# Performance work log

Measured on AMD Instinct MI355X. Metric: run time of the kernel, lower is better.

The kernel has to match this reference:

```python
import jax, jax.numpy as jnp
import numpy as np

N, E, B = 50000, 500000, 500
NODE_IN, EDGE_IN = 64, 16
NODE_OUT, EDGE_OUT = 96, 64
FP_DIM, FP_EMBED = 2048, 128
HIDDEN = [512, 512]
OUT = 256
BN_EPS = 1e-5


def setup_inputs() -> dict:
    key = jax.random.key(0)
    ks = jax.random.split(key, 16)
    inp = {
        "node_feats": jax.random.normal(ks[0], (N, NODE_IN), jnp.float32),
        "edge_feats": jax.random.normal(ks[1], (E, EDGE_IN), jnp.float32),
        "fp_vector": jax.random.uniform(ks[2], (B, FP_DIM), jnp.float32),
        "src": jax.random.randint(ks[3], (E,), 0, N, dtype=jnp.int32),
        "dst": jax.random.randint(ks[4], (E,), 0, N, dtype=jnp.int32),
        "graph_ids": jnp.sort(jax.random.randint(ks[5], (N,), 0, B, dtype=jnp.int32)),
        # mpnn stand-in: single node projection
        "W_mpnn": jax.random.normal(ks[6], (NODE_IN, NODE_OUT), jnp.float32) / np.sqrt(NODE_IN),
        "b_mpnn": jnp.zeros((NODE_OUT,), jnp.float32),
        # project_edge_feats_module: linear edge projection
        "W_edge": jax.random.normal(ks[7], (EDGE_IN, EDGE_OUT), jnp.float32) / np.sqrt(EDGE_IN),
        "b_edge": jnp.zeros((EDGE_OUT,), jnp.float32),
        # FingerprintEncoder: Linear + BatchNorm1d (eval) + ReLU (+Dropout off)
        "W_fp": jax.random.normal(ks[8], (FP_DIM, FP_EMBED), jnp.float32) / np.sqrt(FP_DIM),
        "b_fp": jnp.zeros((FP_EMBED,), jnp.float32),
        "bn_gamma": jnp.ones((FP_EMBED,), jnp.float32),
        "bn_beta": jnp.zeros((FP_EMBED,), jnp.float32),
        "bn_mean": jnp.zeros((FP_EMBED,), jnp.float32),
        "bn_var": jnp.ones((FP_EMBED,), jnp.float32),
    }
    d_in = NODE_OUT + EDGE_OUT + FP_EMBED  # gnn_readout_dim + fp_embed_dim
    dims = [d_in] + HIDDEN + [OUT]
    for i in range(len(dims) - 1):
        inp[f"W_ffn{i}"] = jax.random.normal(ks[9 + i], (dims[i], dims[i + 1]), jnp.float32) / np.sqrt(dims[i])
        inp[f"b_ffn{i}"] = jnp.zeros((dims[i + 1],), jnp.float32)
    return inp


def reference(node_feats, edge_feats, fp_vector, src, dst, graph_ids,
              W_mpnn, b_mpnn, W_edge, b_edge,
              W_fp, b_fp, bn_gamma, bn_beta, bn_mean, bn_var,
              W_ffn0, b_ffn0, W_ffn1, b_ffn1, W_ffn2, b_ffn2):
    # mpnn node encodings [N, NODE_OUT]
    node_emb = node_feats @ W_mpnn + b_mpnn
    # projected edge embeddings [E, EDGE_OUT]
    edge_emb = edge_feats @ W_edge + b_edge
    # message: gather src node emb, concat edge emb -> [E, NODE_OUT+EDGE_OUT]
    msg = jnp.concatenate([node_emb[src], edge_emb], axis=1)
    # reduce: sum messages per destination node -> [N, NODE_OUT+EDGE_OUT]
    node_msg_sum = jax.ops.segment_sum(msg, dst, num_segments=N)
    # global_sum_pooling over nodes per graph -> [B, NODE_OUT+EDGE_OUT]
    mol = jax.ops.segment_sum(node_msg_sum, graph_ids, num_segments=B)
    mol = jax.nn.softmax(mol, axis=1)
    # fingerprint encoder (eval mode: BN uses running stats, dropout off)
    fp = fp_vector @ W_fp + b_fp
    fp = (fp - bn_mean) * jax.lax.rsqrt(bn_var + BN_EPS) * bn_gamma + bn_beta
    fp = jax.nn.relu(fp)
    # combined FFN (dropout off in eval)
    x = jnp.concatenate([mol, fp], axis=1)
    x = jax.nn.relu(x @ W_ffn0 + b_ffn0)
    x = jax.nn.relu(x @ W_ffn1 + b_ffn1)
    return x @ W_ffn2 + b_ffn2
```

## Files before the change

### kernel.cpp

```cpp
#include <hip/hip_runtime.h>
#include <math.h>

#define NODE_IN 64
#define NODE_OUT 96
#define EDGE_IN 16
#define EDGE_OUT 64
#define ACC_W 80
#define NB 500
#define FPD 2048
#define FPE 128
#define XDIM 288
#define BN_EPS 1e-5f
#define HB 2048

__global__ __launch_bounds__(256) void hist_kernel(
    const int* __restrict__ dst, const int* __restrict__ gids,
    int* __restrict__ gkey, int* __restrict__ pbh, int E)
{
    __shared__ int h[NB];
    const int t = threadIdx.x;
    for (int i = t; i < NB; i += 256) h[i] = 0;
    __syncthreads();
    const int e0 = blockIdx.x * HB;
    #pragma unroll
    for (int i = 0; i < HB / 256; ++i) {
        const int e = e0 + i * 256 + t;
        if (e < E) {
            const int g = gids[dst[e]];
            gkey[e] = g;
            atomicAdd(&h[g], 1);
        }
    }
    __syncthreads();
    for (int i = t; i < NB; i += 256)
        pbh[(size_t)blockIdx.x * NB + i] = h[i];
}

__global__ __launch_bounds__(256) void colscan_kernel(
    const int* __restrict__ pbh, int* __restrict__ pcs,
    int* __restrict__ gsum, int nblk)
{
    __shared__ int s[256];
    const int g = blockIdx.x;
    const int t = threadIdx.x;
    const int v0 = (t < nblk) ? pbh[(size_t)t * NB + g] : 0;
    s[t] = v0;
    __syncthreads();
    for (int d = 1; d < 256; d <<= 1) {
        const int v = (t >= d) ? s[t - d] : 0;
        __syncthreads();
        s[t] += v;
        __syncthreads();
    }
    if (t < nblk) pcs[(size_t)t * NB + g] = s[t] - v0;
    if (t == 255) gsum[g] = s[255];
}

__global__ __launch_bounds__(512) void gscan_kernel(
    const int* __restrict__ gsum, int* __restrict__ offs, int* __restrict__ tot)
{
    __shared__ int s[512];
    const int t = threadIdx.x;
    const int v0 = (t < NB) ? gsum[t] : 0;
    s[t] = v0;
    __syncthreads();
    for (int d = 1; d < 512; d <<= 1) {
        const int v = (t >= d) ? s[t - d] : 0;
        __syncthreads();
        s[t] += v;
        __syncthreads();
    }
    if (t < NB) {
        offs[t] = s[t] - v0;
        tot[t]  = v0;
    }
}

__global__ __launch_bounds__(256) void scatter2_kernel(
    const int* __restrict__ gkey, const int* __restrict__ src,
    const int* __restrict__ pcs, const int* __restrict__ offs,
    int* __restrict__ ssrc, int* __restrict__ seid, int E)
{
    __shared__ int h[NB];
    __shared__ int basel[NB];
    const int t = threadIdx.x;
    for (int i = t; i < NB; i += 256) {
        h[i] = 0;
        basel[i] = offs[i] + pcs[(size_t)blockIdx.x * NB + i];
    }
    __syncthreads();
    const int e0 = blockIdx.x * HB;
    #pragma unroll
    for (int i = 0; i < HB / 256; ++i) {
        const int e = e0 + i * 256 + t;
        if (e < E) {
            const int g = gkey[e];
            const int r = atomicAdd(&h[g], 1);
            const int p = basel[g] + r;
            ssrc[p] = src[e];
            seid[p] = e;
        }
    }
}

__global__ __launch_bounds__(1024) void graph_accum(
    const int* __restrict__ ssrc, const int* __restrict__ seid,
    const float* __restrict__ nf, const float* __restrict__ ef,
    const int* __restrict__ offs, const int* __restrict__ tot,
    const float* __restrict__ Wm, const float* __restrict__ bm,
    const float* __restrict__ We, const float* __restrict__ be,
    float* __restrict__ xbuf, int E)
{
    const int g = blockIdx.x;
    const int t = threadIdx.x;
    const int lane = t & 63;
    const int w = t >> 6;
    const int start = offs[g];
    const int cnt = tot[g];
    const int end = start + cnt;
    const int q = lane >> 4, c = lane & 15;

    __shared__ float sacc[16][ACC_W];
    __shared__ float accRow[ACC_W];
    __shared__ float red[1024];

    float nacc = 0.f;
    float eacc = 0.f;

    for (int p0 = start + w * 64; p0 < end; p0 += 1024) {
        const int lim = min(64, end - p0);
        const int sv = ssrc[min(p0 + lane, E - 1)];
        const int ev = seid[min(p0 + lane, E - 1)];

        #pragma unroll
        for (int u0 = 0; u0 < 64; u0 += 16) {
            float v[16];
            #pragma unroll
            for (int u = 0; u < 16; ++u) {
                const int s = __builtin_amdgcn_readlane(sv, u0 + u);
                v[u] = nf[(size_t)s * NODE_IN + lane];
            }
            #pragma unroll
            for (int u = 0; u < 16; ++u)
                nacc += (u0 + u < lim) ? v[u] : 0.f;
        }

        #pragma unroll
        for (int u0 = 0; u0 < 16; u0 += 8) {
            float w8[8];
            int idx8[8];
            #pragma unroll
            for (int u = 0; u < 8; ++u) {
                const int idx = (u0 + u) * 4 + q;
                const int eid = __shfl(ev, idx);
                idx8[u] = idx;
                w8[u] = ef[(size_t)eid * EDGE_IN + c];
            }
            #pragma unroll
            for (int u = 0; u < 8; ++u)
                eacc += (idx8[u] < lim) ? w8[u] : 0.f;
        }
    }

    if (lane < NODE_IN) sacc[w][lane] = nacc;
    eacc += __shfl_xor(eacc, 16);
    eacc += __shfl_xor(eacc, 32);
    if (lane < EDGE_IN) sacc[w][NODE_IN + lane] = eacc;
    __syncthreads();
    if (t < ACC_W) {
        float s = 0.f;
        #pragma unroll
        for (int w2 = 0; w2 < 16; ++w2) s += sacc[w2][t];
        accRow[t] = s;
    }
    __syncthreads();

    const float cntf = (float)cnt;
    float mr = 0.f;
    if (t < 96) {
        float m2 = 0.f;
        for (int k = 0; k < NODE_IN; ++k) m2 = fmaf(accRow[k], Wm[k * NODE_OUT + t], m2);
        mr = m2 + cntf * bm[t];
    } else if (t < 160) {
        const int j = t - 96;
        float m2 = 0.f;
        for (int k = 0; k < EDGE_IN; ++k) m2 = fmaf(accRow[NODE_IN + k], We[k * EDGE_OUT + j], m2);
        mr = m2 + cntf * be[j];
    }

    red[t] = (t < 160) ? mr : -1e30f;
    __syncthreads();
    for (int st = 512; st > 0; st >>= 1) {
        if (t < st) red[t] = fmaxf(red[t], red[t + st]);
        __syncthreads();
    }
    const float mx = red[0];
    __syncthreads();
    const float evx = (t < 160) ? expf(mr - mx) : 0.f;
    red[t] = evx;
    __syncthreads();
    for (int st = 512; st > 0; st >>= 1) {
        if (t < st) red[t] += red[t + st];
        __syncthreads();
    }
    if (t < 160) xbuf[(size_t)g * XDIM + t] = evx / red[0];
}

__global__ __launch_bounds__(1024) void fp_kernel(
    const float* __restrict__ fpv, const float* __restrict__ Wf,
    const float* __restrict__ bf, const float* __restrict__ gam,
    const float* __restrict__ bet, const float* __restrict__ mu,
    const float* __restrict__ var, float* __restrict__ xbuf)
{
    __shared__ float part[7][4][FPE];
    const int t = threadIdx.x;
    const int j  = t & 127;
    const int kh = __builtin_amdgcn_readfirstlane(t >> 7);
    const int r0 = blockIdx.x * 4;
    const int k0 = kh * 256;

    const float* __restrict__ xp0 = fpv + (size_t)(r0 + 0) * FPD + k0;
    const float* __restrict__ xp1 = fpv + (size_t)(r0 + 1) * FPD + k0;
    const float* __restrict__ xp2 = fpv + (size_t)(r0 + 2) * FPD + k0;
    const float* __restrict__ xp3 = fpv + (size_t)(r0 + 3) * FPD + k0;
    const float* __restrict__ wp  = Wf + (size_t)k0 * FPE + j;

    float a0 = 0.f, a1 = 0.f, a2 = 0.f, a3 = 0.f;
    for (int k = 0; k < 256; k += 8) {
        #pragma unroll
        for (int u = 0; u < 8; ++u) {
            const float w = wp[(size_t)(k + u) * FPE];
            a0 = fmaf(xp0[k + u], w, a0);
            a1 = fmaf(xp1[k + u], w, a1);
            a2 = fmaf(xp2[k + u], w, a2);
            a3 = fmaf(xp3[k + u], w, a3);
        }
    }
    if (kh > 0) {
        part[kh - 1][0][j] = a0; part[kh - 1][1][j] = a1;
        part[kh - 1][2][j] = a2; part[kh - 1][3][j] = a3;
    }
    __syncthreads();
    if (kh == 0) {
        #pragma unroll
        for (int qd = 0; qd < 7; ++qd) {
            a0 += part[qd][0][j]; a1 += part[qd][1][j];
            a2 += part[qd][2][j]; a3 += part[qd][3][j];
        }
        const float sc = rsqrtf(var[j] + BN_EPS) * gam[j];
        const float sh = bet[j] - mu[j] * sc;
        const float bj = bf[j];
        xbuf[(size_t)(r0 + 0) * XDIM + 160 + j] = fmaxf(fmaf(a0 + bj, sc, sh), 0.f);
        xbuf[(size_t)(r0 + 1) * XDIM + 160 + j] = fmaxf(fmaf(a1 + bj, sc, sh), 0.f);
        xbuf[(size_t)(r0 + 2) * XDIM + 160 + j] = fmaxf(fmaf(a2 + bj, sc, sh), 0.f);
        xbuf[(size_t)(r0 + 3) * XDIM + 160 + j] = fmaxf(fmaf(a3 + bj, sc, sh), 0.f);
    }
}

template<int NO, int KS>
__global__ __launch_bounds__(1024) void ffn_split(
    const float* __restrict__ X, const float* __restrict__ W,
    const float* __restrict__ bias, float* __restrict__ Y,
    int Bv, int Ni, int doRelu)
{
    __shared__ float part[KS - 1][4][NO];
    const int t = threadIdx.x;
    const int col = t % NO;
    const int ks = __builtin_amdgcn_readfirstlane(t / NO);
    const int r0 = blockIdx.x * 4;
    const int kchunk = Ni / KS;
    const int k0 = ks * kchunk;

    const float* __restrict__ xp0 = X + (size_t)(r0 + 0) * Ni + k0;
    const float* __restrict__ xp1 = X + (size_t)(r0 + 1) * Ni + k0;
    const float* __restrict__ xp2 = X + (size_t)(r0 + 2) * Ni + k0;
    const float* __restrict__ xp3 = X + (size_t)(r0 + 3) * Ni + k0;
    const float* __restrict__ wp  = W + (size_t)k0 * NO + col;

    float a0 = 0.f, a1 = 0.f, a2 = 0.f, a3 = 0.f;
    for (int k = 0; k < kchunk; k += 8) {
        #pragma unroll
        for (int u = 0; u < 8; ++u) {
            const float w = wp[(size_t)(k + u) * NO];
            a0 = fmaf(xp0[k + u], w, a0);
            a1 = fmaf(xp1[k + u], w, a1);
            a2 = fmaf(xp2[k + u], w, a2);
            a3 = fmaf(xp3[k + u], w, a3);
        }
    }
    if (ks > 0) {
        part[ks - 1][0][col] = a0; part[ks - 1][1][col] = a1;
        part[ks - 1][2][col] = a2; part[ks - 1][3][col] = a3;
    }
    __syncthreads();
    if (ks == 0) {
        #pragma unroll
        for (int qd = 0; qd < KS - 1; ++qd) {
            a0 += part[qd][0][col]; a1 += part[qd][1][col];
            a2 += part[qd][2][col]; a3 += part[qd][3][col];
        }
        const float bv = bias[col];
        float o0 = a0 + bv, o1 = a1 + bv, o2 = a2 + bv, o3 = a3 + bv;
        if (doRelu) {
            o0 = fmaxf(o0, 0.f); o1 = fmaxf(o1, 0.f);
            o2 = fmaxf(o2, 0.f); o3 = fmaxf(o3, 0.f);
        }
        Y[(size_t)(r0 + 0) * NO + col] = o0;
        if (r0 + 1 < Bv) Y[(size_t)(r0 + 1) * NO + col] = o1;
        if (r0 + 2 < Bv) Y[(size_t)(r0 + 2) * NO + col] = o2;
        if (r0 + 3 < Bv) Y[(size_t)(r0 + 3) * NO + col] = o3;
    }
}

extern "C" void kernel_launch(void* const* d_in, const int* in_sizes, int n_in,
                              void* d_out, int out_size, void* d_ws, size_t ws_size,
                              hipStream_t stream)
{
    const float* node_feats = (const float*)d_in[0];
    const float* edge_feats = (const float*)d_in[1];
    const float* fpv        = (const float*)d_in[2];
    const int*   src        = (const int*)d_in[3];
    const int*   dst        = (const int*)d_in[4];
    const int*   gids       = (const int*)d_in[5];
    const float* Wm  = (const float*)d_in[6];
    const float* bm  = (const float*)d_in[7];
    const float* We  = (const float*)d_in[8];
    const float* be  = (const float*)d_in[9];
    const float* Wf  = (const float*)d_in[10];
    const float* bf  = (const float*)d_in[11];
    const float* gam = (const float*)d_in[12];
    const float* bet = (const float*)d_in[13];
    const float* mu  = (const float*)d_in[14];
    const float* var = (const float*)d_in[15];
    const float* W0  = (const float*)d_in[16];
    const float* b0  = (const float*)d_in[17];
    const float* W1  = (const float*)d_in[18];
    const float* b1  = (const float*)d_in[19];
    const float* W2  = (const float*)d_in[20];
    const float* b2  = (const float*)d_in[21];
    const int E = in_sizes[3];
    const int nblk = (E + HB - 1) / HB;

    float* xbuf  = (float*)d_ws;
    float* h1    = xbuf + (size_t)NB * XDIM;
    float* h2    = h1 + (size_t)NB * 512;
    int*   gkey  = (int*)(h2 + (size_t)NB * 512);
    int*   ssrc  = gkey + E;
    int*   seid  = ssrc + E;
    int*   pbh   = seid + E;
    int*   pcs   = pbh + (size_t)nblk * NB;
    int*   gsum  = pcs + (size_t)nblk * NB;
    int*   offs  = gsum + NB;
    int*   tot   = offs + NB;

    hipLaunchKernelGGL(hist_kernel, dim3(nblk), dim3(256), 0, stream,
                       dst, gids, gkey, pbh, E);
    hipLaunchKernelGGL(colscan_kernel, dim3(NB), dim3(256), 0, stream,
                       pbh, pcs, gsum, nblk);
    hipLaunchKernelGGL(gscan_kernel, dim3(1), dim3(512), 0, stream,
                       gsum, offs, tot);
    hipLaunchKernelGGL(scatter2_kernel, dim3(nblk), dim3(256), 0, stream,
                       gkey, src, pcs, offs, ssrc, seid, E);
    hipLaunchKernelGGL(graph_accum, dim3(NB), dim3(1024), 0, stream,
                       ssrc, seid, node_feats, edge_feats, offs, tot,
                       Wm, bm, We, be, xbuf, E);
    hipLaunchKernelGGL(fp_kernel, dim3(NB / 4), dim3(1024), 0, stream,
                       fpv, Wf, bf, gam, bet, mu, var, xbuf);
    hipLaunchKernelGGL((ffn_split<512, 2>), dim3((NB + 3) / 4), dim3(1024), 0, stream,
                       xbuf, W0, b0, h1, NB, XDIM, 1);
    hipLaunchKernelGGL((ffn_split<512, 2>), dim3((NB + 3) / 4), dim3(1024), 0, stream,
                       h1, W1, b1, h2, NB, 512, 1);
    hipLaunchKernelGGL((ffn_split<256, 4>), dim3((NB + 3) / 4), dim3(1024), 0, stream,
                       h2, W2, b2, (float*)d_out, NB, 512, 0);
}
```

Measured before the change: 113.6 us.

## Accumulate edge features per graph in histogram pass and fuse fingerprint encoder

The histogram kernel now streams edge features contiguously and accumulates them into per-block, per-graph shared-memory partial sums, written to a new workspace buffer. This removes the sorted edge-id array and the random gather of edge features in the graph accumulation kernel. The fingerprint encoder is merged into the graph accumulation launch as extra blocks, saving one kernel launch and letting the two overlap. In exchange it adds shared-memory float atomics, a 32KB shared array per histogram block, and a strided reduction over all block partials for each graph.

```diff
diff --git a/kernel.cpp b/kernel.cpp
--- a/kernel.cpp
+++ b/kernel.cpp
@@ -13,27 +13,51 @@
 #define BN_EPS 1e-5f
 #define HB 2048
 
-__global__ __launch_bounds__(256) void hist_kernel(
+__global__ __launch_bounds__(512) void hist_kernel(
     const int* __restrict__ dst, const int* __restrict__ gids,
-    int* __restrict__ gkey, int* __restrict__ pbh, int E)
-{
-    __shared__ int h[NB];
-    const int t = threadIdx.x;
-    for (int i = t; i < NB; i += 256) h[i] = 0;
-    __syncthreads();
+    const float* __restrict__ ef,
+    int* __restrict__ gkey, int* __restrict__ pbh, float* __restrict__ pfe, int E)
+{
+    __shared__ int   h[NB];
+    __shared__ float facc[NB * EDGE_IN];
+    const int t = threadIdx.x;
+    for (int i = t; i < NB; i += 512) h[i] = 0;
+    for (int i = t; i < NB * EDGE_IN; i += 512) facc[i] = 0.f;
+    __syncthreads();
+
+    const int lane = t & 63;
+    const int w = t >> 6;
+    const int q = lane >> 4, c = lane & 15;
     const int e0 = blockIdx.x * HB;
-    #pragma unroll
-    for (int i = 0; i < HB / 256; ++i) {
-        const int e = e0 + i * 256 + t;
+
+    for (int b = w; b < HB / 64; b += 8) {
+        const int eb = e0 + b * 64;
+        const int e = eb + lane;
+        int g = -1;
         if (e < E) {
-            const int g = gids[dst[e]];
+            g = gids[dst[e]];
             gkey[e] = g;
             atomicAdd(&h[g], 1);
         }
-    }
-    __syncthreads();
-    for (int i = t; i < NB; i += 256)
+        #pragma unroll
+        for (int k0 = 0; k0 < 16; k0 += 8) {
+            float v[8]; int gq[8];
+            #pragma unroll
+            for (int u = 0; u < 8; ++u) {
+                const int idx = (k0 + u) * 4 + q;
+                gq[u] = __shfl(g, idx);
+                v[u] = (gq[u] >= 0) ? ef[(size_t)(eb + idx) * EDGE_IN + c] : 0.f;
+            }
+            #pragma unroll
+            for (int u = 0; u < 8; ++u)
+                if (gq[u] >= 0) atomicAdd(&facc[gq[u] * EDGE_IN + c], v[u]);
+        }
+    }
+    __syncthreads();
+    for (int i = t; i < NB; i += 512)
         pbh[(size_t)blockIdx.x * NB + i] = h[i];
+    for (int i = t; i < NB * EDGE_IN; i += 512)
+        pfe[(size_t)blockIdx.x * (NB * EDGE_IN) + i] = facc[i];
 }
 
 __global__ __launch_bounds__(256) void colscan_kernel(
@@ -76,62 +100,115 @@
     }
 }
 
-__global__ __launch_bounds__(256) void scatter2_kernel(
+__global__ __launch_bounds__(512) void scatter2_kernel(
     const int* __restrict__ gkey, const int* __restrict__ src,
     const int* __restrict__ pcs, const int* __restrict__ offs,
-    int* __restrict__ ssrc, int* __restrict__ seid, int E)
+    int* __restrict__ ssrc, int E)
 {
     __shared__ int h[NB];
     __shared__ int basel[NB];
     const int t = threadIdx.x;
-    for (int i = t; i < NB; i += 256) {
+    for (int i = t; i < NB; i += 512) {
         h[i] = 0;
         basel[i] = offs[i] + pcs[(size_t)blockIdx.x * NB + i];
     }
     __syncthreads();
     const int e0 = blockIdx.x * HB;
     #pragma unroll
-    for (int i = 0; i < HB / 256; ++i) {
-        const int e = e0 + i * 256 + t;
+    for (int i = 0; i < HB / 512; ++i) {
+        const int e = e0 + i * 512 + t;
         if (e < E) {
             const int g = gkey[e];
             const int r = atomicAdd(&h[g], 1);
-            const int p = basel[g] + r;
-            ssrc[p] = src[e];
-            seid[p] = e;
-        }
-    }
-}
-
-__global__ __launch_bounds__(1024) void graph_accum(
-    const int* __restrict__ ssrc, const int* __restrict__ seid,
-    const float* __restrict__ nf, const float* __restrict__ ef,
-    const int* __restrict__ offs, const int* __restrict__ tot,
+            ssrc[basel[g] + r] = src[e];
+        }
+    }
+}
+
+__global__ __launch_bounds__(1024) void fused_kernel(
+    const int* __restrict__ ssrc, const float* __restrict__ nf,
+    const float* __restrict__ pfe, const int* __restrict__ offs,
+    const int* __restrict__ tot, int nblk,
     const float* __restrict__ Wm, const float* __restrict__ bm,
     const float* __restrict__ We, const float* __restrict__ be,
+    const float* __restrict__ fpv, const float* __restrict__ Wf,
+    const float* __restrict__ bf, const float* __restrict__ gam,
+    const float* __restrict__ bet, const float* __restrict__ mu,
+    const float* __restrict__ var,
     float* __restrict__ xbuf, int E)
 {
+    __shared__ float sacc[16][NODE_IN];
+    __shared__ float epart[16][EDGE_IN];
+    __shared__ float accRow[ACC_W];
+    __shared__ float red[1024];
+    __shared__ float part[7][4][FPE];
+
+    const int t = threadIdx.x;
+
+    if (blockIdx.x >= NB) {
+        const int j  = t & 127;
+        const int kh = __builtin_amdgcn_readfirstlane(t >> 7);
+        const int r0 = (blockIdx.x - NB) * 4;
+        const int k0 = kh * 256;
+
+        const float* __restrict__ xp0 = fpv + (size_t)(r0 + 0) * FPD + k0;
+        const float* __restrict__ xp1 = fpv + (size_t)(r0 + 1) * FPD + k0;
+        const float* __restrict__ xp2 = fpv + (size_t)(r0 + 2) * FPD + k0;
+        const float* __restrict__ xp3 = fpv + (size_t)(r0 + 3) * FPD + k0;
+        const float* __restrict__ wp  = Wf + (size_t)k0 * FPE + j;
+
+        float a0 = 0.f, a1 = 0.f, a2 = 0.f, a3 = 0.f;
+        for (int k = 0; k < 256; k += 8) {
+            #pragma unroll
+            for (int u = 0; u < 8; ++u) {
+                const float w = wp[(size_t)(k + u) * FPE];
+                a0 = fmaf(xp0[k + u], w, a0);
+                a1 = fmaf(xp1[k + u], w, a1);
+                a2 = fmaf(xp2[k + u], w, a2);
+                a3 = fmaf(xp3[k + u], w, a3);
+            }
+        }
+        if (kh > 0) {
+            part[kh - 1][0][j] = a0; part[kh - 1][1][j] = a1;
+            part[kh - 1][2][j] = a2; part[kh - 1][3][j] = a3;
+        }
+        __syncthreads();
+        if (kh == 0) {
+            #pragma unroll
+            for (int qd = 0; qd < 7; ++qd) {
+                a0 += part[qd][0][j]; a1 += part[qd][1][j];
+                a2 += part[qd][2][j]; a3 += part[qd][3][j];
+            }
+            const float sc = rsqrtf(var[j] + BN_EPS) * gam[j];
+            const float sh = bet[j] - mu[j] * sc;
+            const float bj = bf[j];
+            xbuf[(size_t)(r0 + 0) * XDIM + 160 + j] = fmaxf(fmaf(a0 + bj, sc, sh), 0.f);
+            xbuf[(size_t)(r0 + 1) * XDIM + 160 + j] = fmaxf(fmaf(a1 + bj, sc, sh), 0.f);
+            xbuf[(size_t)(r0 + 2) * XDIM + 160 + j] = fmaxf(fmaf(a2 + bj, sc, sh), 0.f);
+            xbuf[(size_t)(r0 + 3) * XDIM + 160 + j] = fmaxf(fmaf(a3 + bj, sc, sh), 0.f);
+        }
+        return;
+    }
+
     const int g = blockIdx.x;
-    const int t = threadIdx.x;
     const int lane = t & 63;
     const int w = t >> 6;
     const int start = offs[g];
     const int cnt = tot[g];
     const int end = start + cnt;
-    const int q = lane >> 4, c = lane & 15;
-
-    __shared__ float sacc[16][ACC_W];
-    __shared__ float accRow[ACC_W];
-    __shared__ float red[1024];
+
+    if (t < 256) {
+        const int c = t & 15, ch = t >> 4;
+        float s = 0.f;
+        for (int b = ch; b < nblk; b += 16)
+            s += pfe[(size_t)b * (NB * EDGE_IN) + g * EDGE_IN + c];
+        epart[ch][c] = s;
+    }
 
     float nacc = 0.f;
-    float eacc = 0.f;
-
     for (int p0 = start + w * 64; p0 < end; p0 += 1024) {
         const int lim = min(64, end - p0);
         const int sv = ssrc[min(p0 + lane, E - 1)];
-        const int ev = seid[min(p0 + lane, E - 1)];
-
         #pragma unroll
         for (int u0 = 0; u0 < 64; u0 += 16) {
             float v[16];
@@ -144,33 +221,20 @@
             for (int u = 0; u < 16; ++u)
                 nacc += (u0 + u < lim) ? v[u] : 0.f;
         }
-
-        #pragma unroll
-        for (int u0 = 0; u0 < 16; u0 += 8) {
-            float w8[8];
-            int idx8[8];
-            #pragma unroll
-            for (int u = 0; u < 8; ++u) {
-                const int idx = (u0 + u) * 4 + q;
-                const int eid = __shfl(ev, idx);
-                idx8[u] = idx;
-                w8[u] = ef[(size_t)eid * EDGE_IN + c];
-            }
-            #pragma unroll
-            for (int u = 0; u < 8; ++u)
-                eacc += (idx8[u] < lim) ? w8[u] : 0.f;
-        }
-    }
-
-    if (lane < NODE_IN) sacc[w][lane] = nacc;
-    eacc += __shfl_xor(eacc, 16);
-    eacc += __shfl_xor(eacc, 32);
-    if (lane < EDGE_IN) sacc[w][NODE_IN + lane] = eacc;
-    __syncthreads();
-    if (t < ACC_W) {
+    }
+    sacc[w][lane] = nacc;
+    __syncthreads();
+
+    if (t < NODE_IN) {
         float s = 0.f;
         #pragma unroll
         for (int w2 = 0; w2 < 16; ++w2) s += sacc[w2][t];
+        accRow[t] = s;
+    } else if (t < ACC_W) {
+        const int c = t - NODE_IN;
+        float s = 0.f;
+        #pragma unroll
+        for (int ch = 0; ch < 16; ++ch) s += epart[ch][c];
         accRow[t] = s;
     }
     __syncthreads();
@@ -204,57 +268,6 @@
         __syncthreads();
     }
     if (t < 160) xbuf[(size_t)g * XDIM + t] = evx / red[0];
-}
-
-__global__ __launch_bounds__(1024) void fp_kernel(
-    const float* __restrict__ fpv, const float* __restrict__ Wf,
-    const float* __restrict__ bf, const float* __restrict__ gam,
-    const float* __restrict__ bet, const float* __restrict__ mu,
-    const float* __restrict__ var, float* __restrict__ xbuf)
-{
-    __shared__ float part[7][4][FPE];
-    const int t = threadIdx.x;
-    const int j  = t & 127;
-    const int kh = __builtin_amdgcn_readfirstlane(t >> 7);
-    const int r0 = blockIdx.x * 4;
-    const int k0 = kh * 256;
-
-    const float* __restrict__ xp0 = fpv + (size_t)(r0 + 0) * FPD + k0;
-    const float* __restrict__ xp1 = fpv + (size_t)(r0 + 1) * FPD + k0;
-    const float* __restrict__ xp2 = fpv + (size_t)(r0 + 2) * FPD + k0;
-    const float* __restrict__ xp3 = fpv + (size_t)(r0 + 3) * FPD + k0;
-    const float* __restrict__ wp  = Wf + (size_t)k0 * FPE + j;
-
-    float a0 = 0.f, a1 = 0.f, a2 = 0.f, a3 = 0.f;
-    for (int k = 0; k < 256; k += 8) {
-        #pragma unroll
-        for (int u = 0; u < 8; ++u) {
-            const float w = wp[(size_t)(k + u) * FPE];
-            a0 = fmaf(xp0[k + u], w, a0);
-            a1 = fmaf(xp1[k + u], w, a1);
-            a2 = fmaf(xp2[k + u], w, a2);
-            a3 = fmaf(xp3[k + u], w, a3);
-        }
-    }
-    if (kh > 0) {
-        part[kh - 1][0][j] = a0; part[kh - 1][1][j] = a1;
-        part[kh - 1][2][j] = a2; part[kh - 1][3][j] = a3;
-    }
-    __syncthreads();
-    if (kh == 0) {
-        #pragma unroll
-        for (int qd = 0; qd < 7; ++qd) {
-            a0 += part[qd][0][j]; a1 += part[qd][1][j];
-            a2 += part[qd][2][j]; a3 += part[qd][3][j];
-        }
-        const float sc = rsqrtf(var[j] + BN_EPS) * gam[j];
-        const float sh = bet[j] - mu[j] * sc;
-        const float bj = bf[j];
-        xbuf[(size_t)(r0 + 0) * XDIM + 160 + j] = fmaxf(fmaf(a0 + bj, sc, sh), 0.f);
-        xbuf[(size_t)(r0 + 1) * XDIM + 160 + j] = fmaxf(fmaf(a1 + bj, sc, sh), 0.f);
-        xbuf[(size_t)(r0 + 2) * XDIM + 160 + j] = fmaxf(fmaf(a2 + bj, sc, sh), 0.f);
-        xbuf[(size_t)(r0 + 3) * XDIM + 160 + j] = fmaxf(fmaf(a3 + bj, sc, sh), 0.f);
-    }
 }
 
 template<int NO, int KS>
@@ -346,26 +359,25 @@
     float* h2    = h1 + (size_t)NB * 512;
     int*   gkey  = (int*)(h2 + (size_t)NB * 512);
     int*   ssrc  = gkey + E;
-    int*   seid  = ssrc + E;
-    int*   pbh   = seid + E;
+    int*   pbh   = ssrc + E;
     int*   pcs   = pbh + (size_t)nblk * NB;
     int*   gsum  = pcs + (size_t)nblk * NB;
     int*   offs  = gsum + NB;
     int*   tot   = offs + NB;
-
-    hipLaunchKernelGGL(hist_kernel, dim3(nblk), dim3(256), 0, stream,
-                       dst, gids, gkey, pbh, E);
+    float* pfe   = (float*)(tot + NB);
+
+    hipLaunchKernelGGL(hist_kernel, dim3(nblk), dim3(512), 0, stream,
+                       dst, gids, edge_feats, gkey, pbh, pfe, E);
     hipLaunchKernelGGL(colscan_kernel, dim3(NB), dim3(256), 0, stream,
                        pbh, pcs, gsum, nblk);
     hipLaunchKernelGGL(gscan_kernel, dim3(1), dim3(512), 0, stream,
                        gsum, offs, tot);
-    hipLaunchKernelGGL(scatter2_kernel, dim3(nblk), dim3(256), 0, stream,
-                       gkey, src, pcs, offs, ssrc, seid, E);
-    hipLaunchKernelGGL(graph_accum, dim3(NB), dim3(1024), 0, stream,
-                       ssrc, seid, node_feats, edge_feats, offs, tot,
-                       Wm, bm, We, be, xbuf, E);
-    hipLaunchKernelGGL(fp_kernel, dim3(NB / 4), dim3(1024), 0, stream,
-                       fpv, Wf, bf, gam, bet, mu, var, xbuf);
+    hipLaunchKernelGGL(scatter2_kernel, dim3(nblk), dim3(512), 0, stream,
+                       gkey, src, pcs, offs, ssrc, E);
+    hipLaunchKernelGGL(fused_kernel, dim3(NB + NB / 4), dim3(1024), 0, stream,
+                       ssrc, node_feats, pfe, offs, tot, nblk,
+                       Wm, bm, We, be,
+                       fpv, Wf, bf, gam, bet, mu, var, xbuf, E);
     hipLaunchKernelGGL((ffn_split<512, 2>), dim3((NB + 3) / 4), dim3(1024), 0, stream,
                        xbuf, W0, b0, h1, NB, XDIM, 1);
     hipLaunchKernelGGL((ffn_split<512, 2>), dim3((NB + 3) / 4), dim3(1024), 0, stream,
```

After: 146.6 us. +29.0%, slower.

## Fuse fingerprint encoder into histogram kernel and shrink per-block edge tile

Applied to the files above, without the earlier changes.

The fingerprint Linear+BN+ReLU blocks are appended to the histogram launch, so the fp matmul overlaps the edge-histogram phase and one kernel launch is removed. The histogram and scatter blocks now use 1024 threads with one edge per thread (HB 1024), which doubles the block count to 489. The column scan is widened to 512 threads to cover that count. The cost is a larger per-block partial histogram array and a longer scan. A small guard on the shared accumulator write is also removed.

```diff
diff --git a/kernel.cpp b/kernel.cpp
--- a/kernel.cpp
+++ b/kernel.cpp
@@ -11,49 +11,96 @@
 #define FPE 128
 #define XDIM 288
 #define BN_EPS 1e-5f
-#define HB 2048
-
-__global__ __launch_bounds__(256) void hist_kernel(
+#define HB 1024
+
+__global__ __launch_bounds__(1024) void hist_fp_kernel(
     const int* __restrict__ dst, const int* __restrict__ gids,
-    int* __restrict__ gkey, int* __restrict__ pbh, int E)
-{
-    __shared__ int h[NB];
-    const int t = threadIdx.x;
-    for (int i = t; i < NB; i += 256) h[i] = 0;
-    __syncthreads();
-    const int e0 = blockIdx.x * HB;
-    #pragma unroll
-    for (int i = 0; i < HB / 256; ++i) {
-        const int e = e0 + i * 256 + t;
-        if (e < E) {
-            const int g = gids[dst[e]];
-            gkey[e] = g;
-            atomicAdd(&h[g], 1);
-        }
-    }
-    __syncthreads();
-    for (int i = t; i < NB; i += 256)
+    int* __restrict__ gkey, int* __restrict__ pbh, int nblk,
+    const float* __restrict__ fpv, const float* __restrict__ Wf,
+    const float* __restrict__ bf, const float* __restrict__ gam,
+    const float* __restrict__ bet, const float* __restrict__ mu,
+    const float* __restrict__ var, float* __restrict__ xbuf, int E)
+{
+    __shared__ int   h[NB];
+    __shared__ float part[7][4][FPE];
+    const int t = threadIdx.x;
+
+    if (blockIdx.x >= nblk) {
+        const int j  = t & 127;
+        const int kh = __builtin_amdgcn_readfirstlane(t >> 7);
+        const int r0 = (blockIdx.x - nblk) * 4;
+        const int k0 = kh * 256;
+
+        const float* __restrict__ xp0 = fpv + (size_t)(r0 + 0) * FPD + k0;
+        const float* __restrict__ xp1 = fpv + (size_t)(r0 + 1) * FPD + k0;
+        const float* __restrict__ xp2 = fpv + (size_t)(r0 + 2) * FPD + k0;
+        const float* __restrict__ xp3 = fpv + (size_t)(r0 + 3) * FPD + k0;
+        const float* __restrict__ wp  = Wf + (size_t)k0 * FPE + j;
+
+        float a0 = 0.f, a1 = 0.f, a2 = 0.f, a3 = 0.f;
+        for (int k = 0; k < 256; k += 8) {
+            #pragma unroll
+            for (int u = 0; u < 8; ++u) {
+                const float w = wp[(size_t)(k + u) * FPE];
+                a0 = fmaf(xp0[k + u], w, a0);
+                a1 = fmaf(xp1[k + u], w, a1);
+                a2 = fmaf(xp2[k + u], w, a2);
+                a3 = fmaf(xp3[k + u], w, a3);
+            }
+        }
+        if (kh > 0) {
+            part[kh - 1][0][j] = a0; part[kh - 1][1][j] = a1;
+            part[kh - 1][2][j] = a2; part[kh - 1][3][j] = a3;
+        }
+        __syncthreads();
+        if (kh == 0) {
+            #pragma unroll
+            for (int qd = 0; qd < 7; ++qd) {
+                a0 += part[qd][0][j]; a1 += part[qd][1][j];
+                a2 += part[qd][2][j]; a3 += part[qd][3][j];
+            }
+            const float sc = rsqrtf(var[j] + BN_EPS) * gam[j];
+            const float sh = bet[j] - mu[j] * sc;
+            const float bj = bf[j];
+            xbuf[(size_t)(r0 + 0) * XDIM + 160 + j] = fmaxf(fmaf(a0 + bj, sc, sh), 0.f);
+            xbuf[(size_t)(r0 + 1) * XDIM + 160 + j] = fmaxf(fmaf(a1 + bj, sc, sh), 0.f);
+            xbuf[(size_t)(r0 + 2) * XDIM + 160 + j] = fmaxf(fmaf(a2 + bj, sc, sh), 0.f);
+            xbuf[(size_t)(r0 + 3) * XDIM + 160 + j] = fmaxf(fmaf(a3 + bj, sc, sh), 0.f);
+        }
+        return;
+    }
+
+    for (int i = t; i < NB; i += 1024) h[i] = 0;
+    __syncthreads();
+    const int e = blockIdx.x * HB + t;
+    if (e < E) {
+        const int g = gids[dst[e]];
+        gkey[e] = g;
+        atomicAdd(&h[g], 1);
+    }
+    __syncthreads();
+    for (int i = t; i < NB; i += 1024)
         pbh[(size_t)blockIdx.x * NB + i] = h[i];
 }
 
-__global__ __launch_bounds__(256) void colscan_kernel(
+__global__ __launch_bounds__(512) void colscan_kernel(
     const int* __restrict__ pbh, int* __restrict__ pcs,
     int* __restrict__ gsum, int nblk)
 {
-    __shared__ int s[256];
+    __shared__ int s[512];
     const int g = blockIdx.x;
     const int t = threadIdx.x;
     const int v0 = (t < nblk) ? pbh[(size_t)t * NB + g] : 0;
     s[t] = v0;
     __syncthreads();
-    for (int d = 1; d < 256; d <<= 1) {
+    for (int d = 1; d < 512; d <<= 1) {
         const int v = (t >= d) ? s[t - d] : 0;
         __syncthreads();
         s[t] += v;
         __syncthreads();
     }
     if (t < nblk) pcs[(size_t)t * NB + g] = s[t] - v0;
-    if (t == 255) gsum[g] = s[255];
+    if (t == 511) gsum[g] = s[511];
 }
 
 __global__ __launch_bounds__(512) void gscan_kernel(
@@ -76,7 +123,7 @@
     }
 }
 
-__global__ __launch_bounds__(256) void scatter2_kernel(
+__global__ __launch_bounds__(1024) void scatter2_kernel(
     const int* __restrict__ gkey, const int* __restrict__ src,
     const int* __restrict__ pcs, const int* __restrict__ offs,
     int* __restrict__ ssrc, int* __restrict__ seid, int E)
@@ -84,22 +131,18 @@
     __shared__ int h[NB];
     __shared__ int basel[NB];
     const int t = threadIdx.x;
-    for (int i = t; i < NB; i += 256) {
+    for (int i = t; i < NB; i += 1024) {
         h[i] = 0;
         basel[i] = offs[i] + pcs[(size_t)blockIdx.x * NB + i];
     }
     __syncthreads();
-    const int e0 = blockIdx.x * HB;
-    #pragma unroll
-    for (int i = 0; i < HB / 256; ++i) {
-        const int e = e0 + i * 256 + t;
-        if (e < E) {
-            const int g = gkey[e];
-            const int r = atomicAdd(&h[g], 1);
-            const int p = basel[g] + r;
-            ssrc[p] = src[e];
-            seid[p] = e;
-        }
+    const int e = blockIdx.x * HB + t;
+    if (e < E) {
+        const int g = gkey[e];
+        const int r = atomicAdd(&h[g], 1);
+        const int p = basel[g] + r;
+        ssrc[p] = src[e];
+        seid[p] = e;
     }
 }
 
@@ -162,7 +205,7 @@
         }
     }
 
-    if (lane < NODE_IN) sacc[w][lane] = nacc;
+    sacc[w][lane] = nacc;
     eacc += __shfl_xor(eacc, 16);
     eacc += __shfl_xor(eacc, 32);
     if (lane < EDGE_IN) sacc[w][NODE_IN + lane] = eacc;
@@ -204,57 +247,6 @@
         __syncthreads();
     }
     if (t < 160) xbuf[(size_t)g * XDIM + t] = evx / red[0];
-}
-
-__global__ __launch_bounds__(1024) void fp_kernel(
-    const float* __restrict__ fpv, const float* __restrict__ Wf,
-    const float* __restrict__ bf, const float* __restrict__ gam,
-    const float* __restrict__ bet, const float* __restrict__ mu,
-    const float* __restrict__ var, float* __restrict__ xbuf)
-{
-    __shared__ float part[7][4][FPE];
-    const int t = threadIdx.x;
-    const int j  = t & 127;
-    const int kh = __builtin_amdgcn_readfirstlane(t >> 7);
-    const int r0 = blockIdx.x * 4;
-    const int k0 = kh * 256;
-
-    const float* __restrict__ xp0 = fpv + (size_t)(r0 + 0) * FPD + k0;
-    const float* __restrict__ xp1 = fpv + (size_t)(r0 + 1) * FPD + k0;
-    const float* __restrict__ xp2 = fpv + (size_t)(r0 + 2) * FPD + k0;
-    const float* __restrict__ xp3 = fpv + (size_t)(r0 + 3) * FPD + k0;
-    const float* __restrict__ wp  = Wf + (size_t)k0 * FPE + j;
-
-    float a0 = 0.f, a1 = 0.f, a2 = 0.f, a3 = 0.f;
-    for (int k = 0; k < 256; k += 8) {
-        #pragma unroll
-        for (int u = 0; u < 8; ++u) {
-            const float w = wp[(size_t)(k + u) * FPE];
-            a0 = fmaf(xp0[k + u], w, a0);
-            a1 = fmaf(xp1[k + u], w, a1);
-            a2 = fmaf(xp2[k + u], w, a2);
-            a3 = fmaf(xp3[k + u], w, a3);
-        }
-    }
-    if (kh > 0) {
-        part[kh - 1][0][j] = a0; part[kh - 1][1][j] = a1;
-        part[kh - 1][2][j] = a2; part[kh - 1][3][j] = a3;
-    }
-    __syncthreads();
-    if (kh == 0) {
-        #pragma unroll
-        for (int qd = 0; qd < 7; ++qd) {
-            a0 += part[qd][0][j]; a1 += part[qd][1][j];
-            a2 += part[qd][2][j]; a3 += part[qd][3][j];
-        }
-        const float sc = rsqrtf(var[j] + BN_EPS) * gam[j];
-        const float sh = bet[j] - mu[j] * sc;
-        const float bj = bf[j];
-        xbuf[(size_t)(r0 + 0) * XDIM + 160 + j] = fmaxf(fmaf(a0 + bj, sc, sh), 0.f);
-        xbuf[(size_t)(r0 + 1) * XDIM + 160 + j] = fmaxf(fmaf(a1 + bj, sc, sh), 0.f);
-        xbuf[(size_t)(r0 + 2) * XDIM + 160 + j] = fmaxf(fmaf(a2 + bj, sc, sh), 0.f);
-        xbuf[(size_t)(r0 + 3) * XDIM + 160 + j] = fmaxf(fmaf(a3 + bj, sc, sh), 0.f);
-    }
 }
 
 template<int NO, int KS>
@@ -353,19 +345,18 @@
     int*   offs  = gsum + NB;
     int*   tot   = offs + NB;
 
-    hipLaunchKernelGGL(hist_kernel, dim3(nblk), dim3(256), 0, stream,
-                       dst, gids, gkey, pbh, E);
-    hipLaunchKernelGGL(colscan_kernel, dim3(NB), dim3(256), 0, stream,
+    hipLaunchKernelGGL(hist_fp_kernel, dim3(nblk + NB / 4), dim3(1024), 0, stream,
+                       dst, gids, gkey, pbh, nblk,
+                       fpv, Wf, bf, gam, bet, mu, var, xbuf, E);
+    hipLaunchKernelGGL(colscan_kernel, dim3(NB), dim3(512), 0, stream,
                        pbh, pcs, gsum, nblk);
     hipLaunchKernelGGL(gscan_kernel, dim3(1), dim3(512), 0, stream,
                        gsum, offs, tot);
-    hipLaunchKernelGGL(scatter2_kernel, dim3(nblk), dim3(256), 0, stream,
+    hipLaunchKernelGGL(scatter2_kernel, dim3(nblk), dim3(1024), 0, stream,
                        gkey, src, pcs, offs, ssrc, seid, E);
     hipLaunchKernelGGL(graph_accum, dim3(NB), dim3(1024), 0, stream,
                        ssrc, seid, node_feats, edge_feats, offs, tot,
                        Wm, bm, We, be, xbuf, E);
-    hipLaunchKernelGGL(fp_kernel, dim3(NB / 4), dim3(1024), 0, stream,
-                       fpv, Wf, bf, gam, bet, mu, var, xbuf);
     hipLaunchKernelGGL((ffn_split<512, 2>), dim3((NB + 3) / 4), dim3(1024), 0, stream,
                        xbuf, W0, b0, h1, NB, XDIM, 1);
     hipLaunchKernelGGL((ffn_split<512, 2>), dim3((NB + 3) / 4), dim3(1024), 0, stream,
```

Result: slower. 116.7 us (+2.7%).
